# Optimization experiments

Measured on AMD Instinct MI355X. Metric: run time of the kernel, lower is better.

## Reference

```python
import jax, jax.numpy as jnp
import numpy as np

B, D, M = 256, 8, 6  # batch, path dimension, signature depth


def setup_inputs() -> dict:
    key = jax.random.key(0)
    k1, k2 = jax.random.split(key)
    siglen = sum(D ** k for k in range(1, M + 1))  # 299592
    x = jax.random.normal(k1, (B, siglen), dtype=jnp.float32)
    # scales kept positive-ish and away from 0, like realistic path scalings
    y = jax.random.uniform(k2, (B, D), dtype=jnp.float32) + 0.5
    return {"x": x, "y": y, "m": M}


def reference(x, y, m):
    """iisignature.sigscale: level-k signature term S_{i1..ik} -> S_{i1..ik} * prod_j y[i_j].

    x: [B, siglen] flattened signature, levels 1..m concatenated, each level k
       stored as d^k entries in row-major (lexicographic word) order.
    y: [B, d] per-sample per-coordinate scale.
    """
    b, d = y.shape
    outs = []
    off = 0
    f = y  # level-1 scale factors, [B, d^1]
    for k in range(1, m + 1):
        n = d ** k
        outs.append(x[:, off:off + n] * f)
        off += n
        if k < m:
            # extend word factors: f[(i1..ik, j)] = f[(i1..ik)] * y[j]
            f = (f[:, :, None] * y[:, None, :]).reshape(b, d ** (k + 1))
    return jnp.concatenate(outs, axis=1)
```

## Files before the change

### kernel.cpp

```cpp
#include <hip/hip_runtime.h>


#define SIGLEN 299592
#define NQ     74898


__global__ __launch_bounds__(256) void sigscale_kernel(
    const float* __restrict__ x,
    const float* __restrict__ y,
    float* __restrict__ out)
{
    __shared__ __align__(16) float f1[8];
    __shared__ float f2[64];
    __shared__ float f3[512];

    const int b   = blockIdx.y;
    const int tid = threadIdx.x;

    if (tid < 8) f1[tid] = y[b * 8 + tid];
    __syncthreads();
    if (tid < 64) f2[tid] = f1[tid >> 3] * f1[tid & 7];
    __syncthreads();
    for (int i = tid; i < 512; i += 256) f3[i] = f2[i >> 3] * f1[i & 7];
    __syncthreads();

    const float4* __restrict__ xr   = reinterpret_cast<const float4*>(x + (size_t)b * SIGLEN);
    float4* __restrict__       orow = reinterpret_cast<float4*>(out + (size_t)b * SIGLEN);

    const int stride = gridDim.x * blockDim.x;
    for (int q = blockIdx.x * blockDim.x + tid; q < NQ; q += stride) {
        float4 v = xr[q];
        const int pos = q << 2;
        int n;
        float g;
        if (pos >= 37448) {
            n = pos - 37448;
            const int p = n >> 3;
            g = f3[p >> 6] * f2[p & 63];
        } else if (pos >= 4680) {
            n = pos - 4680;
            const int p = n >> 3;
            g = f3[p >> 3] * f1[p & 7];
        } else if (pos >= 584) {
            n = pos - 584;
            g = f3[n >> 3];
        } else if (pos >= 72) {
            n = pos - 72;
            g = f2[n >> 3];
        } else if (pos >= 8) {
            n = pos - 8;
            g = f1[n >> 3];
        } else {
            n = pos;
            g = 1.0f;
        }
        const float* yl = &f1[n & 4];
        float4 r;
        r.x = v.x * g * yl[0];
        r.y = v.y * g * yl[1];
        r.z = v.z * g * yl[2];
        r.w = v.w * g * yl[3];
        orow[q] = r;
    }
}

extern "C" void kernel_launch(void* const* d_in, const int* in_sizes, int n_in,
                              void* d_out, int out_size, void* d_ws, size_t ws_size,
                              hipStream_t stream) {
    const float* x = (const float*)d_in[0];
    const float* y = (const float*)d_in[1];
    float* out = (float*)d_out;

    dim3 grid(16, 256);
    sigscale_kernel<<<grid, 256, 0, stream>>>(x, y, out);
}
```

Measured before the change: 142.3 us.

## Align rows to cache lines, unroll 4x with nontemporal vector loads and stores

Each row's start is shifted by a per-batch quad offset so the main loop's accesses line up with 128-byte cache lines. A single thread block handles the misaligned head. The main loop is unrolled four ways with independent nontemporal float4 loads and stores to raise memory-level parallelism and avoid polluting the cache. The per-coordinate y factors now come from registers instead of LDS, and the grid is halved to 8 blocks per row. The risks are lower occupancy from the smaller grid and extra per-iteration branching in the scale lookup.

```diff
diff --git a/kernel.cpp b/kernel.cpp
--- a/kernel.cpp
+++ b/kernel.cpp
@@ -4,6 +4,31 @@
 #define SIGLEN 299592
 #define NQ     74898
 
+typedef float f4 __attribute__((ext_vector_type(4)));
+
+__device__ __forceinline__ float quad_g(int q,
+                                        const float* __restrict__ f1,
+                                        const float* __restrict__ f2,
+                                        const float* __restrict__ f3,
+                                        int& nout) {
+    const int pos = q << 2;
+    int n; float g;
+    if (pos >= 37448) {
+        n = pos - 37448; const int p = n >> 3; g = f3[p >> 6] * f2[p & 63];
+    } else if (pos >= 4680) {
+        n = pos - 4680;  const int p = n >> 3; g = f3[p >> 3] * f1[p & 7];
+    } else if (pos >= 584) {
+        n = pos - 584;   g = f3[n >> 3];
+    } else if (pos >= 72) {
+        n = pos - 72;    g = f2[n >> 3];
+    } else if (pos >= 8) {
+        n = pos - 8;     g = f1[n >> 3];
+    } else {
+        n = pos;         g = 1.0f;
+    }
+    nout = n;
+    return g;
+}
 
 __global__ __launch_bounds__(256) void sigscale_kernel(
     const float* __restrict__ x,
@@ -24,43 +49,55 @@
     for (int i = tid; i < 512; i += 256) f3[i] = f2[i >> 3] * f1[i & 7];
     __syncthreads();
 
-    const float4* __restrict__ xr   = reinterpret_cast<const float4*>(x + (size_t)b * SIGLEN);
-    float4* __restrict__       orow = reinterpret_cast<float4*>(out + (size_t)b * SIGLEN);
+    const f4 ylo = *reinterpret_cast<const f4*>(&f1[0]);
+    const f4 yhi = *reinterpret_cast<const f4*>(&f1[4]);
 
-    const int stride = gridDim.x * blockDim.x;
-    for (int q = blockIdx.x * blockDim.x + tid; q < NQ; q += stride) {
-        float4 v = xr[q];
-        const int pos = q << 2;
-        int n;
-        float g;
-        if (pos >= 37448) {
-            n = pos - 37448;
-            const int p = n >> 3;
-            g = f3[p >> 6] * f2[p & 63];
-        } else if (pos >= 4680) {
-            n = pos - 4680;
-            const int p = n >> 3;
-            g = f3[p >> 3] * f1[p & 7];
-        } else if (pos >= 584) {
-            n = pos - 584;
-            g = f3[n >> 3];
-        } else if (pos >= 72) {
-            n = pos - 72;
-            g = f2[n >> 3];
-        } else if (pos >= 8) {
-            n = pos - 8;
-            g = f1[n >> 3];
-        } else {
-            n = pos;
-            g = 1.0f;
-        }
-        const float* yl = &f1[n & 4];
-        float4 r;
-        r.x = v.x * g * yl[0];
-        r.y = v.y * g * yl[1];
-        r.z = v.z * g * yl[2];
-        r.w = v.w * g * yl[3];
-        orow[q] = r;
+    const f4* __restrict__ xr   = reinterpret_cast<const f4*>(x + (size_t)b * SIGLEN);
+    f4* __restrict__       orow = reinterpret_cast<f4*>(out + (size_t)b * SIGLEN);
+
+    const int s = (-(b << 1)) & 7;
+
+    if (blockIdx.x == 0 && tid < s) {
+        const int q = tid;
+        int n; const float g = quad_g(q, f1, f2, f3, n);
+        const f4 yl = (n & 4) ? yhi : ylo;
+        const f4 v = xr[q];
+        orow[q] = v * g * yl;
+    }
+
+    int q = s + blockIdx.x * 256 + tid;
+
+    for (; q < NQ - 6144; q += 8192) {
+        const int q0 = q, q1 = q + 2048, q2 = q + 4096, q3 = q + 6144;
+        const f4 v0 = __builtin_nontemporal_load(&xr[q0]);
+        const f4 v1 = __builtin_nontemporal_load(&xr[q1]);
+        const f4 v2 = __builtin_nontemporal_load(&xr[q2]);
+        const f4 v3 = __builtin_nontemporal_load(&xr[q3]);
+        int n0, n1, n2, n3;
+        const float g0 = quad_g(q0, f1, f2, f3, n0);
+        const float g1 = quad_g(q1, f1, f2, f3, n1);
+        const float g2 = quad_g(q2, f1, f2, f3, n2);
+        const float g3 = quad_g(q3, f1, f2, f3, n3);
+        const f4 a0 = (n0 & 4) ? yhi : ylo;
+        const f4 a1 = (n1 & 4) ? yhi : ylo;
+        const f4 a2 = (n2 & 4) ? yhi : ylo;
+        const f4 a3 = (n3 & 4) ? yhi : ylo;
+        const f4 r0 = v0 * g0 * a0;
+        const f4 r1 = v1 * g1 * a1;
+        const f4 r2 = v2 * g2 * a2;
+        const f4 r3 = v3 * g3 * a3;
+        __builtin_nontemporal_store(r0, &orow[q0]);
+        __builtin_nontemporal_store(r1, &orow[q1]);
+        __builtin_nontemporal_store(r2, &orow[q2]);
+        __builtin_nontemporal_store(r3, &orow[q3]);
+    }
+
+    for (; q < NQ; q += 2048) {
+        int n; const float g = quad_g(q, f1, f2, f3, n);
+        const f4 yl = (n & 4) ? yhi : ylo;
+        const f4 v = __builtin_nontemporal_load(&xr[q]);
+        const f4 r = v * g * yl;
+        __builtin_nontemporal_store(r, &orow[q]);
     }
 }
 
@@ -71,6 +108,6 @@
     const float* y = (const float*)d_in[1];
     float* out = (float*)d_out;
 
-    dim3 grid(16, 256);
+    dim3 grid(8, 256);
     sigscale_kernel<<<grid, 256, 0, stream>>>(x, y, out);
 }
```

Measured after the change: 123.8 us. -13.0%, faster.
